# Optimization experiments

Hardware: AMD Instinct MI355X
Metric: run time of the kernel (lower is better)

Reference implementation:

```python
import jax, jax.numpy as jnp
import numpy as np

TOP_K = 2


def setup_inputs() -> dict:
    key = jax.random.key(0)
    k0, k1, k2, k3 = jax.random.split(key, 4)
    T, H, E, I = 512, 2048, 16, 1024  # tokens, hidden, experts, intermediate
    return {
        "hidden_states": jax.random.normal(k0, (T, H), jnp.float32),
        "router_weight": jax.random.normal(k1, (E, H), jnp.float32) * 0.02,
        "w13": jax.random.normal(k2, (E, H, 2 * I), jnp.float32) * 0.02,  # fused gate+up
        "w2": jax.random.normal(k3, (E, I, H), jnp.float32) * 0.02,        # down proj
    }


def reference(hidden_states, router_weight, w13, w2):
    x = hidden_states                                   # [T, H]
    E = router_weight.shape[0]
    # Router: linear (no bias) -> softmax -> top-k -> renormalize
    logits = x @ router_weight.T                        # [T, E]
    probs = jax.nn.softmax(logits, axis=-1)
    vals, idx = jax.lax.top_k(probs, TOP_K)             # [T, K]
    vals = vals / jnp.sum(vals, axis=-1, keepdims=True)
    # Dense combine weights [T, E]: zero except the top-k experts per token
    cw = jnp.sum(jax.nn.one_hot(idx, E, dtype=x.dtype) * vals[..., None], axis=1)
    # Scan over experts; each expert runs a SwiGLU MLP over all tokens,
    # scaled by its (mostly-zero) combine weight. Keeps peak memory at [T, I].
    def body(acc, params):
        w13_e, w2_e, cw_e = params                      # [H,2I], [I,H], [T]
        g, u = jnp.split(x @ w13_e, 2, axis=-1)         # [T, I] each
        acc = acc + cw_e[:, None] * ((jax.nn.silu(g) * u) @ w2_e)
        return acc, None
    out, _ = jax.lax.scan(body, jnp.zeros_like(x), (w13, w2, cw.T))
    return out
```

## Files before the change

### kernel.cpp

```cpp
#include <hip/hip_runtime.h>

#define T_TOK 512
#define HID   2048
#define NEXP  16
#define IDIM  1024
#define KC    64

typedef __attribute__((ext_vector_type(8))) short bf16x8;
typedef __attribute__((ext_vector_type(4))) float f32x4;
typedef __attribute__((ext_vector_type(4))) float float4v;

__device__ __forceinline__ unsigned short f2bf(float f) {
    union { float f; unsigned u; } v; v.f = f;
    return (unsigned short)((v.u + 0x7FFFu + ((v.u >> 16) & 1u)) >> 16);
}

__device__ __forceinline__ unsigned pack2(float lo, float hi) {
    return (unsigned)f2bf(lo) | ((unsigned)f2bf(hi) << 16);
}

__device__ __forceinline__ bf16x8 pack8(const float* s) {
    bf16x8 r;
#pragma unroll
    for (int i = 0; i < 8; ++i) r[i] = (short)f2bf(s[i]);
    return r;
}

__global__ __launch_bounds__(256) void router_kernel(
    const float* __restrict__ x, const float* __restrict__ rw,
    int* __restrict__ cnt, int* __restrict__ tok,
    int* __restrict__ rowid, float* __restrict__ wt,
    unsigned short* __restrict__ xb)
{
    int t = blockIdx.x;
    int tid = threadIdx.x;
    const float* xr = x + (size_t)t * HID;

    {
        int c = tid * 8;
        float4v a = *(const float4v*)(xr + c);
        float4v b = *(const float4v*)(xr + c + 4);
        float tmp[8];
#pragma unroll
        for (int i = 0; i < 4; ++i) { tmp[i] = a[i]; tmp[4 + i] = b[i]; }
        *(bf16x8*)(xb + (size_t)t * HID + c) = pack8(tmp);
    }

    float acc[NEXP];
#pragma unroll
    for (int e = 0; e < NEXP; ++e) acc[e] = 0.f;

    for (int k = tid; k < HID; k += 256) {
        float xv = xr[k];
#pragma unroll
        for (int e = 0; e < NEXP; ++e) acc[e] += xv * rw[e * HID + k];
    }

    __shared__ float red[4][NEXP];
    int lane = tid & 63, wv = tid >> 6;
#pragma unroll
    for (int e = 0; e < NEXP; ++e) {
        float v = acc[e];
#pragma unroll
        for (int off = 32; off > 0; off >>= 1) v += __shfl_down(v, off);
        if (lane == 0) red[wv][e] = v;
    }
    __syncthreads();

    if (tid == 0) {
        float l[NEXP];
        float mx = -1e30f;
#pragma unroll
        for (int e = 0; e < NEXP; ++e) {
            l[e] = red[0][e] + red[1][e] + red[2][e] + red[3][e];
            mx = fmaxf(mx, l[e]);
        }
        float s = 0.f;
#pragma unroll
        for (int e = 0; e < NEXP; ++e) { l[e] = __expf(l[e] - mx); s += l[e]; }
        float inv_s = 1.f / s;
        int i0 = 0; float v0 = -1.f;
        int i1 = 0; float v1 = -2.f;
#pragma unroll
        for (int e = 0; e < NEXP; ++e) {
            float p = l[e] * inv_s;
            if (p > v0)      { v1 = v0; i1 = i0; v0 = p; i0 = e; }
            else if (p > v1) { v1 = p; i1 = e; }
        }
        float inv = 1.f / (v0 + v1);
        int p0 = atomicAdd(&cnt[i0], 1);
        tok[i0 * T_TOK + p0] = t; rowid[i0 * T_TOK + p0] = 2 * t;     wt[i0 * T_TOK + p0] = v0 * inv;
        int p1 = atomicAdd(&cnt[i1], 1);
        tok[i1 * T_TOK + p1] = t; rowid[i1 * T_TOK + p1] = 2 * t + 1; wt[i1 * T_TOK + p1] = v1 * inv;
    }
}

#define LOADW(buf, kk_, stride_) { \
    buf[0] = *(const float4v*)(wsrc + (size_t)((kk_) + kg * 2)     * (stride_)); \
    buf[1] = *(const float4v*)(wsrc + (size_t)((kk_) + kg * 2 + 1) * (stride_)); }

#define STOREW(buf, Wd) { _Pragma("unroll") \
    for (int j2 = 0; j2 < 4; ++j2) { \
        int colw = cg * 4 + j2; \
        *(unsigned*)((char*)(Wd) + ((colw * 128 + kg * 4) ^ ((colw & 7) << 4))) = \
            pack2(buf[0][j2], buf[1][j2]); } }

#define LOADX(buf, kk_) { \
    buf[0] = *(const bf16x8*)(xsrc + (kk_)); \
    buf[1] = *(const bf16x8*)(xsrc + (kk_) + 8); }

#define STOREX(buf, Xd) { \
    *(bf16x8*)((char*)(Xd) + ((xrow * 128 + xq * 32)      ^ xswz)) = buf[0]; \
    *(bf16x8*)((char*)(Xd) + ((xrow * 128 + xq * 32 + 16) ^ xswz)) = buf[1]; }

__global__ __launch_bounds__(512, 4) void gemm1_kernel(
    const unsigned short* __restrict__ xb, const float* __restrict__ w13,
    const int* __restrict__ cnt, const int* __restrict__ tok,
    const int* __restrict__ rowid, const float* __restrict__ wt,
    unsigned short* __restrict__ h)
{
    int bid = blockIdx.x;
    int e  = bid >> 5;
    int c0 = (bid & 31) * 32;
    int n = cnt[e];
    int tid = threadIdx.x;

    __shared__ __align__(16) short Xs[2][128 * KC];
    __shared__ __align__(16) short Ws[2][64 * KC];
    __shared__ int   tks[128];
    __shared__ int   rws[128];
    __shared__ float wts[128];

    const float* wbase = w13 + (size_t)e * HID * (2 * IDIM);

    int cg = tid & 15, kg = tid >> 4;
    const float* wsrc = wbase + ((cg < 8) ? (c0 + cg * 4)
                                          : (IDIM + c0 + (cg - 8) * 4));
    int xrow = tid >> 2, xq = tid & 3;
    int xswz = (xrow & 7) << 4;

    int wave = tid >> 6, lane = tid & 63;
    int lr = lane & 15, lh = lane >> 4;
    int swzA = (lr & 7) << 4;

#define G1_MFMA(Xd, Wd) { if (wave * 16 < nt) { _Pragma("unroll") \
    for (int s = 0; s < 2; ++s) { \
        int kb = (s * 32 + lh * 8) * 2; \
        bf16x8 a = *(const bf16x8*)((char*)(Xd) + (((wave * 16 + lr) * 128 + kb) ^ swzA)); \
        _Pragma("unroll") for (int cf = 0; cf < 2; ++cf) { \
            int colg = cf * 16 + lr; \
            bf16x8 bg = *(const bf16x8*)((char*)(Wd) + ((colg * 128 + kb) ^ swzA)); \
            accG[cf] = __builtin_amdgcn_mfma_f32_16x16x32_bf16(a, bg, accG[cf], 0, 0, 0); \
            bf16x8 bu = *(const bf16x8*)((char*)(Wd) + (((32 + colg) * 128 + kb) ^ swzA)); \
            accU[cf] = __builtin_amdgcn_mfma_f32_16x16x32_bf16(a, bu, accU[cf], 0, 0, 0); \
        } } } }

    for (int t0 = 0; t0 < n; t0 += 128) {
        int nt = min(128, n - t0);
        __syncthreads();
        if (tid < 128) {
            int idx = t0 + min(tid, nt - 1);
            tks[tid] = tok[e * T_TOK + idx];
            rws[tid] = rowid[e * T_TOK + idx];
            wts[tid] = wt[e * T_TOK + idx];
        }
        __syncthreads();

        const unsigned short* xsrc = xb + (size_t)tks[xrow] * HID + xq * 16;

        f32x4 accG[2], accU[2];
#pragma unroll
        for (int i = 0; i < 2; ++i) { accG[i] = (f32x4)0.f; accU[i] = (f32x4)0.f; }

        float4v rWa[2], rWb[2];
        bf16x8 rXa[2], rXb[2];
        LOADW(rWa, 0, 2 * IDIM);  LOADX(rXa, 0);
        LOADW(rWb, KC, 2 * IDIM); LOADX(rXb, KC);
        STOREW(rWa, Ws[0]); STOREX(rXa, Xs[0]);
        __syncthreads();

        for (int p = 0; p < HID / KC; p += 2) {
            int kf0 = (p + 2) * KC, kf1 = (p + 3) * KC;
            if (kf0 < HID) { LOADW(rWa, kf0, 2 * IDIM); LOADX(rXa, kf0); }
            G1_MFMA(Xs[0], Ws[0]);
            STOREW(rWb, Ws[1]); STOREX(rXb, Xs[1]);
            __syncthreads();
            if (kf1 < HID) { LOADW(rWb, kf1, 2 * IDIM); LOADX(rXb, kf1); }
            G1_MFMA(Xs[1], Ws[1]);
            if (kf0 < HID) { STOREW(rWa, Ws[0]); STOREX(rXa, Xs[0]); }
            __syncthreads();
        }

#pragma unroll
        for (int cf = 0; cf < 2; ++cf)
#pragma unroll
            for (int r = 0; r < 4; ++r) {
                int row = wave * 16 + lh * 4 + r;
                if (row < nt) {
                    float g = accG[cf][r], u = accU[cf][r];
                    float sg = g / (1.f + __expf(-g));
                    float v = wts[row] * sg * u;
                    h[(size_t)rws[row] * IDIM + c0 + cf * 16 + lr] = f2bf(v);
                }
            }
    }
}

__global__ __launch_bounds__(512, 4) void gemm2_kernel(
    const unsigned short* __restrict__ h, const float* __restrict__ w2,
    const int* __restrict__ cnt, const int* __restrict__ tok,
    const int* __restrict__ rowid,
    float* __restrict__ out)
{
    int bid = blockIdx.x;
    int e  = bid >> 5;
    int c0 = (bid & 31) * 64;
    int n = cnt[e];
    int tid = threadIdx.x;

    __shared__ __align__(16) short Xs[2][128 * KC];
    __shared__ __align__(16) short Ws[2][64 * KC];
    __shared__ int   tks[128];
    __shared__ int   rws[128];

    const float* wbase = w2 + (size_t)e * IDIM * HID;

    int cg = tid & 15, kg = tid >> 4;
    const float* wsrc = wbase + c0 + cg * 4;
    int xrow = tid >> 2, xq = tid & 3;
    int xswz = (xrow & 7) << 4;

    int wave = tid >> 6, lane = tid & 63;
    int lr = lane & 15, lh = lane >> 4;
    int swzA = (lr & 7) << 4;

#define G2_MFMA(Xd, Wd) { if (wave * 16 < nt) { _Pragma("unroll") \
    for (int s = 0; s < 2; ++s) { \
        int kb = (s * 32 + lh * 8) * 2; \
        bf16x8 a = *(const bf16x8*)((char*)(Xd) + (((wave * 16 + lr) * 128 + kb) ^ swzA)); \
        _Pragma("unroll") for (int cf = 0; cf < 4; ++cf) { \
            int col = cf * 16 + lr; \
            bf16x8 b = *(const bf16x8*)((char*)(Wd) + ((col * 128 + kb) ^ swzA)); \
            acc[cf] = __builtin_amdgcn_mfma_f32_16x16x32_bf16(a, b, acc[cf], 0, 0, 0); \
        } } } }

    for (int t0 = 0; t0 < n; t0 += 128) {
        int nt = min(128, n - t0);
        __syncthreads();
        if (tid < 128) {
            int idx = t0 + min(tid, nt - 1);
            tks[tid] = tok[e * T_TOK + idx];
            rws[tid] = rowid[e * T_TOK + idx];
        }
        __syncthreads();

        const unsigned short* xsrc = h + (size_t)rws[xrow] * IDIM + xq * 16;

        f32x4 acc[4];
#pragma unroll
        for (int i = 0; i < 4; ++i) acc[i] = (f32x4)0.f;

        float4v rWa[2], rWb[2];
        bf16x8 rXa[2], rXb[2];
        LOADW(rWa, 0, HID);  LOADX(rXa, 0);
        LOADW(rWb, KC, HID); LOADX(rXb, KC);
        STOREW(rWa, Ws[0]); STOREX(rXa, Xs[0]);
        __syncthreads();

        for (int p = 0; p < IDIM / KC; p += 2) {
            int kf0 = (p + 2) * KC, kf1 = (p + 3) * KC;
            if (kf0 < IDIM) { LOADW(rWa, kf0, HID); LOADX(rXa, kf0); }
            G2_MFMA(Xs[0], Ws[0]);
            STOREW(rWb, Ws[1]); STOREX(rXb, Xs[1]);
            __syncthreads();
            if (kf1 < IDIM) { LOADW(rWb, kf1, HID); LOADX(rXb, kf1); }
            G2_MFMA(Xs[1], Ws[1]);
            if (kf0 < IDIM) { STOREW(rWa, Ws[0]); STOREX(rXa, Xs[0]); }
            __syncthreads();
        }

#pragma unroll
        for (int cf = 0; cf < 4; ++cf)
#pragma unroll
            for (int r = 0; r < 4; ++r) {
                int row = wave * 16 + lh * 4 + r;
                if (row < nt)
                    atomicAdd(&out[(size_t)tks[row] * HID + c0 + cf * 16 + lr], acc[cf][r]);
            }
    }
}

extern "C" void kernel_launch(void* const* d_in, const int* in_sizes, int n_in,
                              void* d_out, int out_size, void* d_ws, size_t ws_size,
                              hipStream_t stream) {
    const float* x   = (const float*)d_in[0];
    const float* rw  = (const float*)d_in[1];
    const float* w13 = (const float*)d_in[2];
    const float* w2  = (const float*)d_in[3];
    float* out = (float*)d_out;

    int* cnt   = (int*)d_ws;
    int* tok   = cnt + 64;
    int* rowid = tok + NEXP * T_TOK;
    float* wt  = (float*)(rowid + NEXP * T_TOK);
    unsigned short* h  = (unsigned short*)((char*)d_ws + 131072);
    unsigned short* xb = (unsigned short*)((char*)d_ws + 131072 + 2097152);

    hipMemsetAsync(out, 0, (size_t)T_TOK * HID * sizeof(float), stream);
    hipMemsetAsync(cnt, 0, 64 * sizeof(int), stream);

    router_kernel<<<T_TOK, 256, 0, stream>>>(x, rw, cnt, tok, rowid, wt, xb);
    gemm1_kernel<<<512, 512, 0, stream>>>(xb, w13, cnt, tok, rowid, wt, h);
    gemm2_kernel<<<512, 512, 0, stream>>>(h, w2, cnt, tok, rowid, out);
}
```

Baseline: 132.9 us.

## Switch expert GEMMs to 32x32x16 MFMA with 4x2 wave tiling

Both expert GEMM kernels move from 16x16x32 MFMA tiles, where each wave owned 16 rows across all columns, to 32x32x16 MFMA with a 4x2 wave grid. Each wave now computes a 32x32 tile, which cuts LDS fragment reads per MFMA. Weight staging changes from float4 loads across columns to 8 scalar strided loads per thread along K, packed into one 16-byte LDS store. In gemm1 the gate and up halves now sit in different waves, so they are exchanged through an extra shared buffer and barrier before SiLU. This risks less coalesced global weight reads and adds an epilogue sync and extra LDS.

Result: no change. 134.6 us (+1.3%).

```diff
diff --git a/kernel.cpp b/kernel.cpp
--- a/kernel.cpp
+++ b/kernel.cpp
@@ -5,18 +5,15 @@
 #define NEXP  16
 #define IDIM  1024
 #define KC    64
-
-typedef __attribute__((ext_vector_type(8))) short bf16x8;
-typedef __attribute__((ext_vector_type(4))) float f32x4;
-typedef __attribute__((ext_vector_type(4))) float float4v;
+#define WSTRIDE 2048
+
+typedef __attribute__((ext_vector_type(8)))  short bf16x8;
+typedef __attribute__((ext_vector_type(16))) float f32x16;
+typedef __attribute__((ext_vector_type(4)))  float float4v;
 
 __device__ __forceinline__ unsigned short f2bf(float f) {
     union { float f; unsigned u; } v; v.f = f;
     return (unsigned short)((v.u + 0x7FFFu + ((v.u >> 16) & 1u)) >> 16);
-}
-
-__device__ __forceinline__ unsigned pack2(float lo, float hi) {
-    return (unsigned)f2bf(lo) | ((unsigned)f2bf(hi) << 16);
 }
 
 __device__ __forceinline__ bf16x8 pack8(const float* s) {
@@ -95,23 +92,19 @@
     }
 }
 
-#define LOADW(buf, kk_, stride_) { \
-    buf[0] = *(const float4v*)(wsrc + (size_t)((kk_) + kg * 2)     * (stride_)); \
-    buf[1] = *(const float4v*)(wsrc + (size_t)((kk_) + kg * 2 + 1) * (stride_)); }
-
-#define STOREW(buf, Wd) { _Pragma("unroll") \
-    for (int j2 = 0; j2 < 4; ++j2) { \
-        int colw = cg * 4 + j2; \
-        *(unsigned*)((char*)(Wd) + ((colw * 128 + kg * 4) ^ ((colw & 7) << 4))) = \
-            pack2(buf[0][j2], buf[1][j2]); } }
-
-#define LOADX(buf, kk_) { \
-    buf[0] = *(const bf16x8*)(xsrc + (kk_)); \
-    buf[1] = *(const bf16x8*)(xsrc + (kk_) + 8); }
-
-#define STOREX(buf, Xd) { \
-    *(bf16x8*)((char*)(Xd) + ((xrow * 128 + xq * 32)      ^ xswz)) = buf[0]; \
-    *(bf16x8*)((char*)(Xd) + ((xrow * 128 + xq * 32 + 16) ^ xswz)) = buf[1]; }
+#define LOADW(r, kk_) { _Pragma("unroll") for (int j = 0; j < 8; ++j) \
+    r[j] = wsrc[(size_t)((kk_) + kq * 8 + j) * WSTRIDE]; }
+
+#define STOREW(r, bufi) { \
+    *(bf16x8*)((char*)Ws[bufi] + ((wcol * 128 + kq * 16) ^ ((wcol & 7) << 4))) = pack8(r); }
+
+#define LOADX(r, kk_) { \
+    r[0] = *(const bf16x8*)(xsrc + (kk_)); \
+    r[1] = *(const bf16x8*)(xsrc + (kk_) + 8); }
+
+#define STOREX(r, bufi) { \
+    *(bf16x8*)((char*)Xs[bufi] + ((xrow * 128 + xq * 32)      ^ xswz)) = r[0]; \
+    *(bf16x8*)((char*)Xs[bufi] + ((xrow * 128 + xq * 32 + 16) ^ xswz)) = r[1]; }
 
 __global__ __launch_bounds__(512, 4) void gemm1_kernel(
     const unsigned short* __restrict__ xb, const float* __restrict__ w13,
@@ -120,40 +113,38 @@
     unsigned short* __restrict__ h)
 {
     int bid = blockIdx.x;
-    int e  = bid >> 5;
-    int c0 = (bid & 31) * 32;
+    int e   = bid >> 5;
+    int c0h = (bid & 31) * 32;
     int n = cnt[e];
     int tid = threadIdx.x;
 
     __shared__ __align__(16) short Xs[2][128 * KC];
     __shared__ __align__(16) short Ws[2][64 * KC];
+    __shared__ float Ex[4][16][64];
     __shared__ int   tks[128];
     __shared__ int   rws[128];
     __shared__ float wts[128];
 
     const float* wbase = w13 + (size_t)e * HID * (2 * IDIM);
 
-    int cg = tid & 15, kg = tid >> 4;
-    const float* wsrc = wbase + ((cg < 8) ? (c0 + cg * 4)
-                                          : (IDIM + c0 + (cg - 8) * 4));
+    int wcol = tid & 63, kq = tid >> 6;
+    const float* wsrc = wbase + ((wcol < 32) ? (c0h + wcol)
+                                             : (IDIM + c0h + (wcol - 32)));
     int xrow = tid >> 2, xq = tid & 3;
     int xswz = (xrow & 7) << 4;
 
     int wave = tid >> 6, lane = tid & 63;
-    int lr = lane & 15, lh = lane >> 4;
-    int swzA = (lr & 7) << 4;
-
-#define G1_MFMA(Xd, Wd) { if (wave * 16 < nt) { _Pragma("unroll") \
-    for (int s = 0; s < 2; ++s) { \
-        int kb = (s * 32 + lh * 8) * 2; \
-        bf16x8 a = *(const bf16x8*)((char*)(Xd) + (((wave * 16 + lr) * 128 + kb) ^ swzA)); \
-        _Pragma("unroll") for (int cf = 0; cf < 2; ++cf) { \
-            int colg = cf * 16 + lr; \
-            bf16x8 bg = *(const bf16x8*)((char*)(Wd) + ((colg * 128 + kb) ^ swzA)); \
-            accG[cf] = __builtin_amdgcn_mfma_f32_16x16x32_bf16(a, bg, accG[cf], 0, 0, 0); \
-            bf16x8 bu = *(const bf16x8*)((char*)(Wd) + (((32 + colg) * 128 + kb) ^ swzA)); \
-            accU[cf] = __builtin_amdgcn_mfma_f32_16x16x32_bf16(a, bu, accU[cf], 0, 0, 0); \
-        } } } }
+    int wm = wave & 3, wn = wave >> 2;
+    int lrow = lane & 31, lhalf = lane >> 5;
+    int swz = (lrow & 7) << 4;
+
+#define G1_MFMA(bufi) { if (wm * 32 < nt) { _Pragma("unroll") \
+    for (int s = 0; s < 4; ++s) { \
+        int kb = s * 32 + lhalf * 16; \
+        bf16x8 a = *(const bf16x8*)((char*)Xs[bufi] + (((wm * 32 + lrow) * 128 + kb) ^ swz)); \
+        bf16x8 b = *(const bf16x8*)((char*)Ws[bufi] + (((wn * 32 + lrow) * 128 + kb) ^ swz)); \
+        acc = __builtin_amdgcn_mfma_f32_32x32x16_bf16(a, b, acc, 0, 0, 0); \
+    } } }
 
     for (int t0 = 0; t0 < n; t0 += 128) {
         int nt = min(128, n - t0);
@@ -168,41 +159,44 @@
 
         const unsigned short* xsrc = xb + (size_t)tks[xrow] * HID + xq * 16;
 
-        f32x4 accG[2], accU[2];
-#pragma unroll
-        for (int i = 0; i < 2; ++i) { accG[i] = (f32x4)0.f; accU[i] = (f32x4)0.f; }
-
-        float4v rWa[2], rWb[2];
+        f32x16 acc = (f32x16)0.f;
+        float  rWa[8], rWb[8];
         bf16x8 rXa[2], rXb[2];
-        LOADW(rWa, 0, 2 * IDIM);  LOADX(rXa, 0);
-        LOADW(rWb, KC, 2 * IDIM); LOADX(rXb, KC);
-        STOREW(rWa, Ws[0]); STOREX(rXa, Xs[0]);
+
+        LOADW(rWa, 0);  LOADX(rXa, 0);
+        LOADW(rWb, KC); LOADX(rXb, KC);
+        STOREW(rWa, 0); STOREX(rXa, 0);
         __syncthreads();
 
         for (int p = 0; p < HID / KC; p += 2) {
             int kf0 = (p + 2) * KC, kf1 = (p + 3) * KC;
-            if (kf0 < HID) { LOADW(rWa, kf0, 2 * IDIM); LOADX(rXa, kf0); }
-            G1_MFMA(Xs[0], Ws[0]);
-            STOREW(rWb, Ws[1]); STOREX(rXb, Xs[1]);
+            if (kf0 < HID) { LOADW(rWa, kf0); LOADX(rXa, kf0); }
+            G1_MFMA(0);
+            STOREW(rWb, 1); STOREX(rXb, 1);
             __syncthreads();
-            if (kf1 < HID) { LOADW(rWb, kf1, 2 * IDIM); LOADX(rXb, kf1); }
-            G1_MFMA(Xs[1], Ws[1]);
-            if (kf0 < HID) { STOREW(rWa, Ws[0]); STOREX(rXa, Xs[0]); }
+            if (kf1 < HID) { LOADW(rWb, kf1); LOADX(rXb, kf1); }
+            G1_MFMA(1);
+            if (kf0 < HID) { STOREW(rWa, 0); STOREX(rXa, 0); }
             __syncthreads();
         }
 
-#pragma unroll
-        for (int cf = 0; cf < 2; ++cf)
-#pragma unroll
-            for (int r = 0; r < 4; ++r) {
-                int row = wave * 16 + lh * 4 + r;
-                if (row < nt) {
-                    float g = accG[cf][r], u = accU[cf][r];
+        if (wn == 1) {
+#pragma unroll
+            for (int q = 0; q < 16; ++q) Ex[wm][q][lane] = acc[q];
+        }
+        __syncthreads();
+        if (wn == 0) {
+#pragma unroll
+            for (int q = 0; q < 16; ++q) {
+                int r = wm * 32 + (q & 3) + 8 * (q >> 2) + 4 * lhalf;
+                if (r < nt) {
+                    float g = acc[q];
+                    float u = Ex[wm][q][lane];
                     float sg = g / (1.f + __expf(-g));
-                    float v = wts[row] * sg * u;
-                    h[(size_t)rws[row] * IDIM + c0 + cf * 16 + lr] = f2bf(v);
+                    h[(size_t)rws[r] * IDIM + c0h + lrow] = f2bf(wts[r] * sg * u);
                 }
             }
+        }
     }
 }
 
@@ -225,24 +219,23 @@
 
     const float* wbase = w2 + (size_t)e * IDIM * HID;
 
-    int cg = tid & 15, kg = tid >> 4;
-    const float* wsrc = wbase + c0 + cg * 4;
+    int wcol = tid & 63, kq = tid >> 6;
+    const float* wsrc = wbase + c0 + wcol;
     int xrow = tid >> 2, xq = tid & 3;
     int xswz = (xrow & 7) << 4;
 
     int wave = tid >> 6, lane = tid & 63;
-    int lr = lane & 15, lh = lane >> 4;
-    int swzA = (lr & 7) << 4;
-
-#define G2_MFMA(Xd, Wd) { if (wave * 16 < nt) { _Pragma("unroll") \
-    for (int s = 0; s < 2; ++s) { \
-        int kb = (s * 32 + lh * 8) * 2; \
-        bf16x8 a = *(const bf16x8*)((char*)(Xd) + (((wave * 16 + lr) * 128 + kb) ^ swzA)); \
-        _Pragma("unroll") for (int cf = 0; cf < 4; ++cf) { \
-            int col = cf * 16 + lr; \
-            bf16x8 b = *(const bf16x8*)((char*)(Wd) + ((col * 128 + kb) ^ swzA)); \
-            acc[cf] = __builtin_amdgcn_mfma_f32_16x16x32_bf16(a, b, acc[cf], 0, 0, 0); \
-        } } } }
+    int wm = wave & 3, wn = wave >> 2;
+    int lrow = lane & 31, lhalf = lane >> 5;
+    int swz = (lrow & 7) << 4;
+
+#define G2_MFMA(bufi) { if (wm * 32 < nt) { _Pragma("unroll") \
+    for (int s = 0; s < 4; ++s) { \
+        int kb = s * 32 + lhalf * 16; \
+        bf16x8 a = *(const bf16x8*)((char*)Xs[bufi] + (((wm * 32 + lrow) * 128 + kb) ^ swz)); \
+        bf16x8 b = *(const bf16x8*)((char*)Ws[bufi] + (((wn * 32 + lrow) * 128 + kb) ^ swz)); \
+        acc = __builtin_amdgcn_mfma_f32_32x32x16_bf16(a, b, acc, 0, 0, 0); \
+    } } }
 
     for (int t0 = 0; t0 < n; t0 += 128) {
         int nt = min(128, n - t0);
@@ -256,37 +249,33 @@
 
         const unsigned short* xsrc = h + (size_t)rws[xrow] * IDIM + xq * 16;
 
-        f32x4 acc[4];
-#pragma unroll
-        for (int i = 0; i < 4; ++i) acc[i] = (f32x4)0.f;
-
-        float4v rWa[2], rWb[2];
+        f32x16 acc = (f32x16)0.f;
+        float  rWa[8], rWb[8];
         bf16x8 rXa[2], rXb[2];
-        LOADW(rWa, 0, HID);  LOADX(rXa, 0);
-        LOADW(rWb, KC, HID); LOADX(rXb, KC);
-        STOREW(rWa, Ws[0]); STOREX(rXa, Xs[0]);
+
+        LOADW(rWa, 0);  LOADX(rXa, 0);
+        LOADW(rWb, KC); LOADX(rXb, KC);
+        STOREW(rWa, 0); STOREX(rXa, 0);
         __syncthreads();
 
         for (int p = 0; p < IDIM / KC; p += 2) {
             int kf0 = (p + 2) * KC, kf1 = (p + 3) * KC;
-            if (kf0 < IDIM) { LOADW(rWa, kf0, HID); LOADX(rXa, kf0); }
-            G2_MFMA(Xs[0], Ws[0]);
-            STOREW(rWb, Ws[1]); STOREX(rXb, Xs[1]);
+            if (kf0 < IDIM) { LOADW(rWa, kf0); LOADX(rXa, kf0); }
+            G2_MFMA(0);
+            STOREW(rWb, 1); STOREX(rXb, 1);
             __syncthreads();
-            if (kf1 < IDIM) { LOADW(rWb, kf1, HID); LOADX(rXb, kf1); }
-            G2_MFMA(Xs[1], Ws[1]);
-            if (kf0 < IDIM) { STOREW(rWa, Ws[0]); STOREX(rXa, Xs[0]); }
+            if (kf1 < IDIM) { LOADW(rWb, kf1); LOADX(rXb, kf1); }
+            G2_MFMA(1);
+            if (kf0 < IDIM) { STOREW(rWa, 0); STOREX(rXa, 0); }
             __syncthreads();
         }
 
 #pragma unroll
-        for (int cf = 0; cf < 4; ++cf)
-#pragma unroll
-            for (int r = 0; r < 4; ++r) {
-                int row = wave * 16 + lh * 4 + r;
-                if (row < nt)
-                    atomicAdd(&out[(size_t)tks[row] * HID + c0 + cf * 16 + lr], acc[cf][r]);
-            }
+        for (int q = 0; q < 16; ++q) {
+            int r = wm * 32 + (q & 3) + 8 * (q >> 2) + 4 * lhalf;
+            if (r < nt)
+                atomicAdd(&out[(size_t)tks[r] * HID + c0 + wn * 32 + lrow], acc[q]);
+        }
     }
 }
 
```
